# Performance work log

Hardware: AMD Instinct MI355X
Metric: run time of the kernel (lower is better)

The kernel has to match this reference:

```python
import jax, jax.numpy as jnp
import numpy as np

B, N, F_IN = 256, 256, 128
HID, DEPTH = 48, 4
D_OUT = 97                 # sum(latent_dim [32,32,32,1]) = GraphUNet out_channels
K_SORT = 30
C1, C2, KW2 = 16, 32, 5
POOL_LEN = (K_SORT - 2) // 2 + 1        # 15 after maxpool1d(2,2)
DENSE_DIM = (POOL_LEN - KW2 + 1) * C2   # 352
OUT_DIM = 32


def _gcn(x, A, W, b):
    # GCNConv(improved=True): A_hat = A + 2I; out = D^-1/2 A_hat D^-1/2 (x W) + b
    n = A.shape[-1]
    Ah = A + 2.0 * jnp.eye(n, dtype=A.dtype)
    dinv = jax.lax.rsqrt(jnp.sum(Ah, axis=-1))          # deg >= 2 always
    An = dinv[:, :, None] * Ah * dinv[:, None, :]
    return An @ (x @ W) + b


def _augment(A):
    # GraphUNet.augment_adj: add self loops, two-hop (A@A), remove self loops
    n = A.shape[-1]
    eye = jnp.eye(n, dtype=A.dtype)
    A1 = A + eye
    return (A1 @ A1) * (1.0 - eye)


def _topk_pool(x, A, p):
    # TopKPooling(ratio=0.5, nonlinearity=tanh): score = tanh(x.p/||p||)
    Bb, n, _ = x.shape
    score = jnp.tanh((x @ p) / jnp.sqrt(jnp.sum(p * p)))
    k = (n + 1) // 2
    vals, perm = jax.lax.top_k(score, k)                # [B,k]
    bidx = jnp.arange(Bb)[:, None]
    xp = x[bidx, perm] * vals[..., None]                # gate kept nodes by score
    Ap = A[bidx[..., None], perm[:, :, None], perm[:, None, :]]
    return xp, Ap, perm


def _forward(x, A, dW0, db0, dW, db, pool_p, uW, ub, uWl, ubl, c1W, c1b, c2W, c2b, oW, ob):
    act = jax.nn.relu
    # ---- GraphUNet down path ----
    h = act(_gcn(x, A, dW0, db0))
    xs, As, perms = [h], [A], []
    Acur = A
    for i in range(DEPTH):
        A2 = _augment(Acur)
        h, Acur, perm = _topk_pool(h, A2, pool_p[i])
        h = act(_gcn(h, Acur, dW[i], db[i]))
        if i < DEPTH - 1:
            xs.append(h)
            As.append(Acur)
        perms.append(perm)
    # ---- up path with sum skip connections ----
    for i in range(DEPTH):
        j = DEPTH - 1 - i
        res, Aj, perm = xs[j], As[j], perms[j]
        bidx = jnp.arange(res.shape[0])[:, None]
        up = jnp.zeros_like(res).at[bidx, perm].set(h)
        h = res + up
        if i < DEPTH - 1:
            h = act(_gcn(h, Aj, uW[i], ub[i]))
        else:
            h = _gcn(h, Aj, uWl, ubl)                   # [B,N,D_OUT], no act
    # ---- global_sort_pool: sort nodes by last channel desc, keep top K_SORT ----
    _, order = jax.lax.top_k(h[..., -1], K_SORT)
    sp = h[jnp.arange(B)[:, None], order]               # [B,K_SORT,D_OUT]
    # conv1d(1->C1, kernel=stride=D_OUT) on flattened [B,1,K*D] == per-node linear
    y = jax.nn.relu(jnp.einsum('bkd,cd->bck', sp, c1W) + c1b[None, :, None])  # [B,C1,K]
    y = y.reshape(B, C1, POOL_LEN, 2).max(-1)           # maxpool1d(2,2)
    y = jax.lax.conv_general_dilated(y, c2W, (1,), 'VALID',
                                     dimension_numbers=('NCH', 'OIH', 'NCH'))
    y = jax.nn.relu(y + c2b[None, :, None])             # [B,C2,POOL_LEN-KW2+1]
    return jax.nn.relu(y.reshape(B, -1) @ oW + ob)      # relu(relu(.)) == relu(.)


def setup_inputs():
    key = jax.random.key(0)
    ks = jax.random.split(key, 12)
    x = jax.random.normal(ks[0], (B, N, F_IN), dtype=jnp.float32)
    # symmetric binary adjacency, no self loops, avg degree ~15
    u = jax.random.uniform(ks[1], (B, N, N))
    A = (u < 0.03).astype(jnp.float32)
    A = jnp.maximum(A, A.transpose(0, 2, 1)) * (1.0 - jnp.eye(N, dtype=jnp.float32))
    s = lambda f: np.float32(1.0 / np.sqrt(f))
    return dict(
        x=x, A=A,
        dW0=jax.random.normal(ks[2], (F_IN, HID), dtype=jnp.float32) * s(F_IN),
        db0=jnp.zeros((HID,), jnp.float32),
        dW=jax.random.normal(ks[3], (DEPTH, HID, HID), dtype=jnp.float32) * s(HID),
        db=jnp.zeros((DEPTH, HID), jnp.float32),
        pool_p=jax.random.normal(ks[4], (DEPTH, HID), dtype=jnp.float32) * s(HID),
        uW=jax.random.normal(ks[5], (DEPTH - 1, HID, HID), dtype=jnp.float32) * s(HID),
        ub=jnp.zeros((DEPTH - 1, HID), jnp.float32),
        uWl=jax.random.normal(ks[6], (HID, D_OUT), dtype=jnp.float32) * s(HID),
        ubl=jnp.zeros((D_OUT,), jnp.float32),
        c1W=jax.random.normal(ks[7], (C1, D_OUT), dtype=jnp.float32) * s(D_OUT),
        c1b=jnp.zeros((C1,), jnp.float32),
        c2W=jax.random.normal(ks[8], (C2, C1, KW2), dtype=jnp.float32) * s(C1 * KW2),
        c2b=jnp.zeros((C2,), jnp.float32),
        oW=jax.random.normal(ks[9], (DENSE_DIM, OUT_DIM), dtype=jnp.float32) * s(DENSE_DIM),
        ob=jnp.zeros((OUT_DIM,), jnp.float32),
    )


def reference(x, A, dW0, db0, dW, db, pool_p, uW, ub, uWl, ubl, c1W, c1b, c2W, c2b, oW, ob):
    return _forward(x, A, dW0, db0, dW, db, pool_p, uW, ub, uWl, ubl, c1W, c1b, c2W, c2b, oW, ob)
```

## Files before the change

### kernel.cpp

```cpp
#include <hip/hip_runtime.h>
#include <math.h>

#define BATCH 256
#define NNODE 256
#define FIN   128
#define HID   48
#define DOUT  97

#define WOFF_DW0 0
#define WOFF_DW  6144
#define WOFF_UW  18432
#define WOFF_UWL 27648
#define WTOT     34816

typedef __attribute__((ext_vector_type(8))) short bf16x8_t;
typedef __attribute__((ext_vector_type(4))) float f32x4_t;

__device__ inline unsigned short f2bf(float x) {
  unsigned u = __float_as_uint(x);
  u += 0x7fff + ((u >> 16) & 1);
  return (unsigned short)(u >> 16);
}
__device__ inline float bf2f(unsigned short h) {
  return __uint_as_float(((unsigned)h) << 16);
}

template<int L> __device__ inline float grp_sum(float v) {
  #pragma unroll
  for (int o = L >> 1; o > 0; o >>= 1) v += __shfl_xor(v, o);
  return v;
}
template<int L> __device__ inline int grp_isum(int v) {
  #pragma unroll
  for (int o = L >> 1; o > 0; o >>= 1) v += __shfl_xor(v, o);
  return v;
}

__global__ __launch_bounds__(256) void k_prepA(const float* __restrict__ A,
                                               unsigned short* __restrict__ Abf,
                                               float* __restrict__ dinv, int rows) {
  int wid = (blockIdx.x * 256 + threadIdx.x) >> 6;
  int lane = threadIdx.x & 63;
  if (wid >= rows) return;
  const float4* rp = (const float4*)(A + (size_t)wid * 256);
  float4 v = rp[lane];
  unsigned long long pk = (unsigned long long)f2bf(v.x)
                        | ((unsigned long long)f2bf(v.y) << 16)
                        | ((unsigned long long)f2bf(v.z) << 32)
                        | ((unsigned long long)f2bf(v.w) << 48);
  *(unsigned long long*)(Abf + (size_t)wid * 256 + lane * 4) = pk;
  float s = v.x + v.y + v.z + v.w;
  #pragma unroll
  for (int o = 32; o > 0; o >>= 1) s += __shfl_down(s, o);
  if (lane == 0) dinv[wid] = 1.0f / sqrtf(s + 2.0f);
}

__global__ __launch_bounds__(256) void k_splitW3(const float* __restrict__ dW0,
                                                 const float* __restrict__ dW,
                                                 const float* __restrict__ uW,
                                                 const float* __restrict__ uWl,
                                                 unsigned short* __restrict__ Wp) {
  int idx = blockIdx.x * 256 + threadIdx.x;
  if (idx >= WTOT) return;
  float v;
  if (idx < WOFF_DW) {
    int f = idx / 128, kk = idx - f * 128;
    v = dW0[kk * HID + f];
  } else if (idx < WOFF_UW) {
    int r = idx - WOFF_DW;
    int i = r / 3072; r -= i * 3072;
    int f = r / 64, kk = r - f * 64;
    v = (kk < HID) ? dW[((size_t)i * HID + kk) * HID + f] : 0.f;
  } else if (idx < WOFF_UWL) {
    int r = idx - WOFF_UW;
    int i = r / 3072; r -= i * 3072;
    int f = r / 64, kk = r - f * 64;
    v = (kk < HID) ? uW[((size_t)i * HID + kk) * HID + f] : 0.f;
  } else {
    int r = idx - WOFF_UWL;
    int f = r / 64, kk = r - f * 64;
    v = (f < DOUT && kk < HID) ? uWl[(size_t)kk * DOUT + f] : 0.f;
  }
  unsigned short h = f2bf(v);
  float r1 = v - bf2f(h);
  unsigned short m = f2bf(r1);
  float r2 = r1 - bf2f(m);
  unsigned short l = f2bf(r2);
  Wp[idx] = h;
  Wp[idx + WTOT] = m;
  Wp[idx + 2 * WTOT] = l;
}

__global__ __launch_bounds__(1024) void k_big(const float* __restrict__ x,
                                              const unsigned short* __restrict__ Wp0,
                                              const unsigned short* __restrict__ Abf0,
                                              const float* __restrict__ D0,
                                              const float* __restrict__ db0,
                                              float* __restrict__ H0) {
  __shared__ __align__(16) char yt0[24576];
  __shared__ __align__(16) char yt1[24576];
  int b = blockIdx.x, t = threadIdx.x;
  int w = t >> 6, lane = t & 63;
  int r = lane & 15, q = lane >> 4;
  const float* Xb = x + (size_t)b * 256 * 128;
  const float* Db = D0 + (size_t)b * 256;
  {
    int m = w;
    const float* xr = Xb + (size_t)(m * 16 + r) * 128;
    bf16x8_t ah[4], am[4], al[4];
    #pragma unroll
    for (int ks = 0; ks < 4; ks++) {
      int col0 = ks * 32 + q * 8;
      float4 a4 = *(const float4*)(xr + col0);
      float4 b4 = *(const float4*)(xr + col0 + 4);
      float v[8] = {a4.x, a4.y, a4.z, a4.w, b4.x, b4.y, b4.z, b4.w};
      #pragma unroll
      for (int j = 0; j < 8; j++) {
        unsigned short h = f2bf(v[j]); float r1 = v[j] - bf2f(h);
        unsigned short mm = f2bf(r1);  float r2 = r1 - bf2f(mm);
        ah[ks][j] = (short)h; am[ks][j] = (short)mm; al[ks][j] = (short)f2bf(r2);
      }
    }
    int row0 = m * 16 + q * 4;
    float4 dv4 = *(const float4*)(Db + row0);
    float dvv[4] = {dv4.x, dv4.y, dv4.z, dv4.w};
    #pragma unroll
    for (int ft = 0; ft < 3; ft++) {
      int fl = ft * 16 + r;
      const unsigned short* wb = Wp0 + (size_t)fl * 128 + q * 8;
      f32x4_t acc = {0.f, 0.f, 0.f, 0.f};
      #pragma unroll
      for (int ks = 0; ks < 4; ks++) {
        bf16x8_t bh = *(const bf16x8_t*)(wb + ks * 32);
        bf16x8_t bm = *(const bf16x8_t*)(wb + WTOT + ks * 32);
        bf16x8_t bl = *(const bf16x8_t*)(wb + 2 * WTOT + ks * 32);
        acc = __builtin_amdgcn_mfma_f32_16x16x32_bf16(ah[ks], bh, acc, 0, 0, 0);
        acc = __builtin_amdgcn_mfma_f32_16x16x32_bf16(ah[ks], bm, acc, 0, 0, 0);
        acc = __builtin_amdgcn_mfma_f32_16x16x32_bf16(am[ks], bh, acc, 0, 0, 0);
        acc = __builtin_amdgcn_mfma_f32_16x16x32_bf16(am[ks], bm, acc, 0, 0, 0);
        acc = __builtin_amdgcn_mfma_f32_16x16x32_bf16(ah[ks], bl, acc, 0, 0, 0);
        acc = __builtin_amdgcn_mfma_f32_16x16x32_bf16(al[ks], bh, acc, 0, 0, 0);
      }
      #pragma unroll
      for (int reg = 0; reg < 4; reg++) {
        float vv = dvv[reg] * acc[reg];
        unsigned short hi = f2bf(vv);
        unsigned short lo = f2bf(vv - bf2f(hi));
        int byte = (fl * 512 + (row0 + reg) * 2) ^ ((fl & 7) << 4);
        *(unsigned short*)(yt0 + byte) = hi;
        *(unsigned short*)(yt1 + byte) = lo;
      }
    }
  }
  __syncthreads();
  {
    int it = w;
    const unsigned short* ap = Abf0 + ((size_t)b * 256 + it * 16 + r) * 256 + q * 8;
    bf16x8_t af[8];
    #pragma unroll
    for (int ks = 0; ks < 8; ks++) af[ks] = *(const bf16x8_t*)(ap + ks * 32);
    #pragma unroll
    for (int ft = 0; ft < 3; ft++) {
      int fl = ft * 16 + r;
      f32x4_t acc = {0.f, 0.f, 0.f, 0.f};
      #pragma unroll
      for (int ks = 0; ks < 8; ks++) {
        int byte = (fl * 512 + (ks * 32 + q * 8) * 2) ^ ((fl & 7) << 4);
        bf16x8_t bh = *(const bf16x8_t*)(yt0 + byte);
        bf16x8_t bl = *(const bf16x8_t*)(yt1 + byte);
        acc = __builtin_amdgcn_mfma_f32_16x16x32_bf16(af[ks], bh, acc, 0, 0, 0);
        acc = __builtin_amdgcn_mfma_f32_16x16x32_bf16(af[ks], bl, acc, 0, 0, 0);
      }
      float bfv = db0[fl];
      #pragma unroll
      for (int reg = 0; reg < 4; reg++) {
        int rr = it * 16 + q * 4 + reg;
        int sbyte = (fl * 512 + rr * 2) ^ ((fl & 7) << 4);
        float selfv = bf2f(*(const unsigned short*)(yt0 + sbyte))
                    + bf2f(*(const unsigned short*)(yt1 + sbyte));
        float d = Db[rr];
        float v = d * acc[reg] + 2.f * d * selfv + bfv;
        H0[((size_t)b * 256 + rr) * 48 + fl] = fmaxf(v, 0.f);
      }
    }
  }
}

template<int MODE>
__device__ inline void gcn128_phase(const float* __restrict__ Xg,
                                    const unsigned short* __restrict__ Wpl,
                                    const unsigned short* __restrict__ A1,
                                    const float* __restrict__ D1b,
                                    const float* __restrict__ bias,
                                    char* yt0, char* yt1,
                                    float* __restrict__ H1,
                                    float* __restrict__ H0b,
                                    const int* sPerm1, int t) {
  int w = t >> 6, lane = t & 63;
  int r = lane & 15, q = lane >> 4;
  for (int task = w; task < 24; task += 16) {
    int m = task / 3, ft = task - m * 3;
    const float* xr = Xg + (size_t)(m * 16 + r) * 48;
    bf16x8_t ah[2], am[2], al[2];
    #pragma unroll
    for (int ks = 0; ks < 2; ks++) {
      int col0 = ks * 32 + q * 8;
      float v[8];
      if (col0 + 8 <= 48) {
        float4 a4 = *(const float4*)(xr + col0);
        float4 b4 = *(const float4*)(xr + col0 + 4);
        v[0]=a4.x; v[1]=a4.y; v[2]=a4.z; v[3]=a4.w;
        v[4]=b4.x; v[5]=b4.y; v[6]=b4.z; v[7]=b4.w;
      } else {
        #pragma unroll
        for (int j = 0; j < 8; j++) v[j] = (col0 + j < 48) ? xr[col0 + j] : 0.f;
      }
      #pragma unroll
      for (int j = 0; j < 8; j++) {
        unsigned short h = f2bf(v[j]); float r1 = v[j] - bf2f(h);
        unsigned short mm = f2bf(r1);  float r2 = r1 - bf2f(mm);
        ah[ks][j] = (short)h; am[ks][j] = (short)mm; al[ks][j] = (short)f2bf(r2);
      }
    }
    int row0 = m * 16 + q * 4;
    float4 dv4 = *(const float4*)(D1b + row0);
    float dvv[4] = {dv4.x, dv4.y, dv4.z, dv4.w};
    int fl = ft * 16 + r;
    const unsigned short* wb = Wpl + (size_t)fl * 64 + q * 8;
    f32x4_t acc = {0.f, 0.f, 0.f, 0.f};
    #pragma unroll
    for (int ks = 0; ks < 2; ks++) {
      bf16x8_t bh = *(const bf16x8_t*)(wb + ks * 32);
      bf16x8_t bm = *(const bf16x8_t*)(wb + WTOT + ks * 32);
      bf16x8_t bl = *(const bf16x8_t*)(wb + 2 * WTOT + ks * 32);
      acc = __builtin_amdgcn_mfma_f32_16x16x32_bf16(ah[ks], bh, acc, 0, 0, 0);
      acc = __builtin_amdgcn_mfma_f32_16x16x32_bf16(ah[ks], bm, acc, 0, 0, 0);
      acc = __builtin_amdgcn_mfma_f32_16x16x32_bf16(am[ks], bh, acc, 0, 0, 0);
      acc = __builtin_amdgcn_mfma_f32_16x16x32_bf16(am[ks], bm, acc, 0, 0, 0);
      acc = __builtin_amdgcn_mfma_f32_16x16x32_bf16(ah[ks], bl, acc, 0, 0, 0);
      acc = __builtin_amdgcn_mfma_f32_16x16x32_bf16(al[ks], bh, acc, 0, 0, 0);
// ... 88 lines not shown
  for (int g = sub; g < 48; g += LPR) acc += hr[g] * p[g];
  acc = grp_sum<LPR>(acc);
  if (sub == 0) sS[row] = tanhf(acc / sqrtf(pn));
  __syncthreads();
  {
    float v = sS[row];
    int rk = 0;
    for (int j = sub; j < N; j += LPR) {
      float u = sS[j];
      rk += (u > v) || (u == v && j < row);
    }
    rk = grp_isum<LPR>(rk);
    if (sub == 0 && rk < K) perm[rk] = row;
  }
  __syncthreads();
  for (int idx = t; idx < K * 48; idx += 1024) {
    int r = idx / 48, g = idx - r * 48;
    int pi = perm[r];
    hin[idx] = h[pi * 48 + g] * sS[pi];
  }
  for (int idx = t; idx < K * K; idx += 1024) {
    int r = idx / K, c = idx - r * K;
    int pr = perm[r], pc = perm[c];
    const float* ra = A + pr * lda;
    const float* rc = A + pc * lda;
    float a2 = 0.f;
    #pragma unroll 4
    for (int j = 0; j < N; j++) a2 += ra[j] * rc[j];
    float v = a2 + 2.f * ra[pc];
    Ao[r * ldo + c] = (r == c) ? 0.f : v;
  }
  __syncthreads();
  {
    constexpr int LPR2 = 1024 / K;
    constexpr int LG = (LPR2 > 64 ? 64 : LPR2);
    int row2 = t / LPR2, sub2 = t % LPR2;
    float s = 0.f;
    for (int j = sub2; j < K; j += LPR2) s += Ao[row2 * ldo + j];
    s = grp_sum<LG>(s);
    if (sub2 == 0) dout[row2] = 1.0f / sqrtf(s + 2.0f);
  }
  __syncthreads();
}

__device__ inline void scat_phase(const int* perm, const float* src, float* dst,
                                  int k, int t) {
  for (int idx = t; idx < k * 48; idx += 1024) {
    int r = idx / 48, g = idx - r * 48;
    dst[perm[r] * 48 + g] += src[idx];
  }
  __syncthreads();
}

__global__ __launch_bounds__(1024) void k_mid(const unsigned short* __restrict__ Abf0,
                                              unsigned short* __restrict__ Abf1g,
                                              float* __restrict__ H0,
                                              float* __restrict__ H1g,
                                              float* __restrict__ D1g,
                                              const unsigned short* __restrict__ Wp,
                                              const float* __restrict__ dW,
                                              const float* __restrict__ dbv,
                                              const float* __restrict__ pp,
                                              const float* __restrict__ uW,
                                              const float* __restrict__ ub) {
  int b = blockIdx.x, t = threadIdx.x;
  __shared__ __align__(16) char arena[63488];
  __shared__ int sPerm1[128];
  float* H1 = H1g + (size_t)b * 128 * 48;
  float* H0b = H0 + (size_t)b * 256 * 48;
  unsigned short* A1 = Abf1g + (size_t)b * 128 * 128;
  float* D1b = D1g + (size_t)b * 128;

  {
    float* sc = (float*)arena;
    const float* p = pp;
    float pn = 0.f;
    #pragma unroll
    for (int g = 0; g < 48; g++) pn += p[g] * p[g];
    int row = t >> 2, sub = t & 3;
    const float* hr = H0b + (size_t)row * 48;
    float a = 0.f;
    for (int g = sub; g < 48; g += 4) a += hr[g] * p[g];
    a = grp_sum<4>(a);
    if (!sub) sc[row] = tanhf(a / sqrtf(pn));
    __syncthreads();
    float vv = sc[row];
    int rk = 0;
    for (int j = sub; j < 256; j += 4) {
      float u = sc[j];
      rk += (u > vv) || (u == vv && j < row);
    }
    rk = grp_isum<4>(rk);
    if (!sub && rk < 128) sPerm1[rk] = row;
  }
  __syncthreads();

  {
    float* sc = (float*)arena;
    for (int idx = t; idx < 128 * 48; idx += 1024) {
      int rr = idx / 48, g = idx - rr * 48;
      int pi = sPerm1[rr];
      H1[idx] = H0b[(size_t)pi * 48 + g] * sc[pi];
    }
    int w = t >> 6, lane = t & 63;
    int r = lane & 15, q = lane >> 4;
    int it = w >> 1, fh = w & 1;
    int rowA = sPerm1[it * 16 + r];
    const unsigned short* Ab = Abf0 + (size_t)b * 256 * 256;
    const unsigned short* pa = Ab + (size_t)rowA * 256 + q * 8;
    bf16x8_t af[8];
    #pragma unroll
    for (int ks = 0; ks < 8; ks++) {
      bf16x8_t a = *(const bf16x8_t*)(pa + ks * 32);
      int da = rowA - ks * 32 - q * 8;
      #pragma unroll
      for (int e = 0; e < 8; e++) if (da == e) a[e] = (short)0x3F80;
      af[ks] = a;
    }
    for (int ft = fh * 4; ft < fh * 4 + 4; ft++) {
      int rowB = sPerm1[ft * 16 + r];
      const unsigned short* pb = Ab + (size_t)rowB * 256 + q * 8;
      f32x4_t acc = {0.f, 0.f, 0.f, 0.f};
      #pragma unroll
      for (int ks = 0; ks < 8; ks++) {
        bf16x8_t bv = *(const bf16x8_t*)(pb + ks * 32);
        int db_ = rowB - ks * 32 - q * 8;
        #pragma unroll
        for (int e = 0; e < 8; e++) if (db_ == e) bv[e] = (short)0x3F80;
        acc = __builtin_amdgcn_mfma_f32_16x16x32_bf16(af[ks], bv, acc, 0, 0, 0);
      }
      int c = ft * 16 + r;
      #pragma unroll
      for (int reg = 0; reg < 4; reg++) {
        int rr = it * 16 + q * 4 + reg;
        float v = (rr == c) ? 0.f : acc[reg];
        A1[(size_t)rr * 128 + c] = f2bf(v);
      }
    }
  }
  __syncthreads();
  {
    int row = t >> 3, sub = t & 7;
    const unsigned* ar = (const unsigned*)(A1 + (size_t)row * 128);
    float s = 0.f;
    for (int jj = sub; jj < 64; jj += 8) {
      unsigned u = ar[jj];
      s += bf2f((unsigned short)(u & 0xffffu)) + bf2f((unsigned short)(u >> 16));
    }
    s = grp_sum<8>(s);
    if (sub == 0) D1b[row] = 1.0f / sqrtf(s + 2.0f);
  }
  __syncthreads();

  gcn128_phase<0>(H1, Wp + WOFF_DW, A1, D1b, dbv,
                  (char*)arena, (char*)arena + 12288, H1, nullptr, sPerm1, t);

  {
    float* sS  = (float*)(arena);
    int*   sP2 = (int*)(arena + 512);
    int*   sP3 = (int*)(arena + 768);
    int*   sP4 = (int*)(arena + 896);
    float* sD2 = (float*)(arena + 960);
    float* sD3 = (float*)(arena + 1216);
    float* sD4 = (float*)(arena + 1344);
    float* sA2 = (float*)(arena + 1536);
    float* sA3 = (float*)(arena + 18176);
    float* sH2 = (float*)(arena + 22400);
    float* sH3 = (float*)(arena + 34688);
    float* sXW = (float*)(arena + 40832);
    float* hin = (float*)(arena + 53120);
    float* sH4 = (float*)(arena + 59264);
    float* sA4 = (float*)(arena + 62336);

    {
      const float* p = pp + 48;
      float pn = 0.f;
      #pragma unroll
      for (int g = 0; g < 48; g++) pn += p[g] * p[g];
      int row = t >> 3, sub = t & 7;
      const float* hr = H1 + (size_t)row * 48;
      float acc = 0.f;
      for (int g = sub; g < 48; g += 8) acc += hr[g] * p[g];
      acc = grp_sum<8>(acc);
      if (sub == 0) sS[row] = tanhf(acc / sqrtf(pn));
      __syncthreads();
      float v = sS[row];
      int rk = 0;
      for (int j = sub; j < 128; j += 8) {
        float u = sS[j];
        rk += (u > v) || (u == v && j < row);
      }
      rk = grp_isum<8>(rk);
      if (sub == 0 && rk < 64) sP2[rk] = row;
      __syncthreads();
    }
    {
      int w = t >> 6, lane = t & 63;
      int r = lane & 15, q = lane >> 4;
      int it = w >> 2, ft = w & 3;
      int rowA = sP2[it * 16 + r];
      int rowB = sP2[ft * 16 + r];
      const unsigned short* pa = A1 + (size_t)rowA * 128 + q * 8;
      const unsigned short* pb = A1 + (size_t)rowB * 128 + q * 8;
      f32x4_t acc = {0.f, 0.f, 0.f, 0.f};
      #pragma unroll
      for (int k0 = 0; k0 < 128; k0 += 32) {
        bf16x8_t a  = *(const bf16x8_t*)(pa + k0);
        bf16x8_t bv = *(const bf16x8_t*)(pb + k0);
        int daA = rowA - k0 - q * 8;
        int daB = rowB - k0 - q * 8;
        #pragma unroll
        for (int e = 0; e < 8; e++) {
          if (daA == e) a[e] = (short)0x3F80;
          if (daB == e) bv[e] = (short)0x3F80;
        }
        acc = __builtin_amdgcn_mfma_f32_16x16x32_bf16(a, bv, acc, 0, 0, 0);
      }
      int c = ft * 16 + r;
      #pragma unroll
      for (int reg = 0; reg < 4; reg++) {
        int rr = it * 16 + q * 4 + reg;
        sA2[rr * 65 + c] = (rr == c) ? 0.f : acc[reg];
      }
    }
    __syncthreads();
    {
      int row = t >> 4, sub = t & 15;
      float s = 0.f;
      for (int j = sub; j < 64; j += 16) s += sA2[row * 65 + j];
      s = grp_sum<16>(s);
      if (sub == 0) sD2[row] = 1.0f / sqrtf(s + 2.0f);
    }
    __syncthreads();
    for (int idx = t; idx < 64 * 48; idx += 1024) {
      int j = idx / 48, f = idx - j * 48;
      int pi = sP2[j];
      const float* hr = H1 + (size_t)pi * 48;
      const float* W = dW + 2304;
      float a = 0.f;
      #pragma unroll
      for (int g = 0; g < 48; g++) a += hr[g] * W[g * 48 + f];
      sXW[idx] = sD2[j] * sS[pi] * a;
    }
    __syncthreads();
    anxw_phase(sA2, 65, sXW, sD2, dbv + 48, sH2, 64, t);
    __syncthreads();

    pool_aug_phaseT<64, 32>(sH2, pp + 96, sA2, 65, sA3, 33, sS, sP3, hin, sD3, t);
    xw_dphase(hin, dW + 2 * 2304, sD3, sXW, 32, t);
    __syncthreads();
    anxw_phase(sA3, 33, sXW, sD3, dbv + 96, sH3, 32, t);
    __syncthreads();

    pool_aug_phaseT<32, 16>(sH3, pp + 144, sA3, 33, sA4, 17, sS, sP4, hin, sD4, t);
    xw_dphase(hin, dW + 3 * 2304, sD4, sXW, 16, t);
    __syncthreads();
    anxw_phase(sA4, 17, sXW, sD4, dbv + 144, sH4, 16, t);
    __syncthreads();

    scat_phase(sP4, sH4, sH3, 16, t);
    xw_dphase(sH3, uW, sD3, sXW, 32, t);
    __syncthreads();
    anxw_phase(sA3, 33, sXW, sD3, ub, sH3, 32, t);
    __syncthreads();

    scat_phase(sP3, sH3, sH2, 32, t);
    xw_dphase(sH2, uW + 2304, sD2, sXW, 64, t);
    __syncthreads();
    anxw_phase(sA2, 65, sXW, sD2, ub + 48, sH2, 64, t);
    __syncthreads();

    for (int idx = t; idx < 64 * 48; idx += 1024) {
      int r2 = idx / 48, g = idx - r2 * 48;
      H1[(size_t)sP2[r2] * 48 + g] += sH2[idx];
    }
  }
  __syncthreads();

  gcn128_phase<1>(H1, Wp + WOFF_UW + 2 * 3072, A1, D1b, ub + 96,
                  (char*)arena, (char*)arena + 12288, nullptr, H0b, sPerm1, t);
}

__global__ __launch_bounds__(1024) void k_tail(const float* __restrict__ H0,
                                               const unsigned short* __restrict__ Wpl,
                                               const unsigned short* __restrict__ Abf,
                                               const float* __restrict__ dinv,
                                               const float* __restrict__ ubl,
                                               float* __restrict__ sp) {
  int b = blockIdx.x, t = threadIdx.x;
  __shared__ float ydt[16][257];
  __shared__ float sc[256];
  __shared__ int sord[32];
  int w = t >> 6, lane = t & 63;
  int r = lane & 15, q = lane >> 4;
  const float* H0b = H0 + (size_t)b * 256 * 48;
  const float* Db = dinv + (size_t)b * 256;

  bf16x8_t ah[2], am[2], al[2];
  {
    const float* xr = H0b + (size_t)(w * 16 + r) * 48;
    #pragma unroll
    for (int ks = 0; ks < 2; ks++) {
      int col0 = ks * 32 + q * 8;
      float v[8];
      if (col0 + 8 <= 48) {
        float4 a4 = *(const float4*)(xr + col0);
        float4 b4 = *(const float4*)(xr + col0 + 4);
        v[0]=a4.x; v[1]=a4.y; v[2]=a4.z; v[3]=a4.w;
        v[4]=b4.x; v[5]=b4.y; v[6]=b4.z; v[7]=b4.w;
      } else {
        #pragma unroll
        for (int j = 0; j < 8; j++) v[j] = (col0 + j < 48) ? xr[col0 + j] : 0.f;
      }
      #pragma unroll
      for (int j = 0; j < 8; j++) {
        unsigned short h = f2bf(v[j]); float r1 = v[j] - bf2f(h);
        unsigned short mm = f2bf(r1);  float r2 = r1 - bf2f(mm);
        ah[ks][j] = (short)h; am[ks][j] = (short)mm; al[ks][j] = (short)f2bf(r2);
      }
    }
  }
  int row0 = w * 16 + q * 4;
  float4 dv4 = *(const float4*)(Db + row0);
  float dvv[4] = {dv4.x, dv4.y, dv4.z, dv4.w};

  auto stepA = [&](int ft) {
    int fl = ft * 16 + r;
    const unsigned short* wb = Wpl + (size_t)fl * 64 + q * 8;
    f32x4_t acc = {0.f, 0.f, 0.f, 0.f};
    #pragma unroll
    for (int ks = 0; ks < 2; ks++) {
      bf16x8_t bh = *(const bf16x8_t*)(wb + ks * 32);
      bf16x8_t bm = *(const bf16x8_t*)(wb + WTOT + ks * 32);
      bf16x8_t bl = *(const bf16x8_t*)(wb + 2 * WTOT + ks * 32);
      acc = __builtin_amdgcn_mfma_f32_16x16x32_bf16(ah[ks], bh, acc, 0, 0, 0);
      acc = __builtin_amdgcn_mfma_f32_16x16x32_bf16(ah[ks], bm, acc, 0, 0, 0);
      acc = __builtin_amdgcn_mfma_f32_16x16x32_bf16(am[ks], bh, acc, 0, 0, 0);
      acc = __builtin_amdgcn_mfma_f32_16x16x32_bf16(am[ks], bm, acc, 0, 0, 0);
      acc = __builtin_amdgcn_mfma_f32_16x16x32_bf16(ah[ks], bl, acc, 0, 0, 0);
      acc = __builtin_amdgcn_mfma_f32_16x16x32_bf16(al[ks], bh, acc, 0, 0, 0);
    }
    #pragma unroll
    for (int reg = 0; reg < 4; reg++)
      ydt[r][row0 + reg] = dvv[reg] * acc[reg];
  };

  auto stepB = [&](int ft, int nf) {
    int o = t >> 1, sub = t & 1;
    if (o < 30 * nf) {
      int rr = o / nf, f = o - rr * nf;
      int fl = ft * 16 + f;
      int node = sord[rr];
      const unsigned short* ar = Abf + ((size_t)b * 256 + node) * 256 + sub * 128;
      const float* yp = &ydt[f][sub * 128];
      float s = 0.f;
      for (int j = 0; j < 128; j += 2) {
        unsigned u = *(const unsigned*)(ar + j);
        s += bf2f((unsigned short)(u & 0xffffu)) * yp[j]
           + bf2f((unsigned short)(u >> 16)) * yp[j + 1];
      }
      s += __shfl_xor(s, 1);
      if (!sub) {
        float d = Db[node];
        sp[((size_t)b * 30 + rr) * DOUT + fl] = d * s + 2.f * d * ydt[f][node] + ubl[fl];
      }
    }
  };

  stepA(6);
  __syncthreads();
  {
    int i = t >> 2, sub = t & 3;
    const unsigned short* ar = Abf + ((size_t)b * 256 + i) * 256 + sub * 64;
    const float* yp = &ydt[0][sub * 64];
    float s = 0.f;
    for (int j = 0; j < 64; j += 2) {
      unsigned u = *(const unsigned*)(ar + j);
      s += bf2f((unsigned short)(u & 0xffffu)) * yp[j]
         + bf2f((unsigned short)(u >> 16)) * yp[j + 1];
    }
    s = grp_sum<4>(s);
    if (!sub) {
      float d = Db[i];
      sc[i] = d * s + 2.f * d * ydt[0][i];
    }
  }
  __syncthreads();
  {
    int i = t >> 2, sub = t & 3;
    float v = sc[i];
    int rk = 0;
    int j0 = sub * 64;
    for (int j = j0; j < j0 + 64; j++) {
      float u = sc[j];
      rk += (u > v) || (u == v && j < i);
    }
    rk = grp_isum<4>(rk);
    if (!sub && rk < 30) sord[rk] = i;
  }
  __syncthreads();
  stepB(6, 1);
  __syncthreads();
  for (int ft = 0; ft < 6; ft++) {
    stepA(ft);
    __syncthreads();
    stepB(ft, 16);
    __syncthreads();
  }
}

__global__ __launch_bounds__(256) void k_head2(const float* __restrict__ spg,
                                               const float* __restrict__ c1W,
                                               const float* __restrict__ c1b,
                                               const float* __restrict__ c2W,
                                               const float* __restrict__ c2b,
                                               const float* __restrict__ oW,
                                               const float* __restrict__ ob,
                                               float* __restrict__ out) {
  int b = blockIdx.x, t = threadIdx.x;
  __shared__ float sp[30 * 97];
  __shared__ float y1[16 * 30];
  __shared__ float yp[16 * 15];
  __shared__ float yc[32 * 11];
  __shared__ float red[256];
  const float* spb = spg + (size_t)b * 30 * 97;
  for (int idx = t; idx < 30 * 97; idx += 256) sp[idx] = spb[idx];
  __syncthreads();
  for (int idx = t; idx < 16 * 30; idx += 256) {
    int c = idx / 30, kk = idx - c * 30;
    float a = c1b[c];
    for (int d = 0; d < 97; d++) a += sp[kk * 97 + d] * c1W[c * 97 + d];
    y1[c * 30 + kk] = fmaxf(a, 0.f);
  }
  __syncthreads();
  for (int idx = t; idx < 16 * 15; idx += 256) {
    int c = idx / 15, t2 = idx - c * 15;
    yp[idx] = fmaxf(y1[c * 30 + 2 * t2], y1[c * 30 + 2 * t2 + 1]);
  }
  __syncthreads();
  for (int idx = t; idx < 32 * 11; idx += 256) {
    int o = idx / 11, t3 = idx - o * 11;
    float a = c2b[o];
    for (int i2 = 0; i2 < 16; i2++)
      for (int w = 0; w < 5; w++)
        a += yp[i2 * 15 + t3 + w] * c2W[(o * 16 + i2) * 5 + w];
    yc[o * 11 + t3] = fmaxf(a, 0.f);
  }
  __syncthreads();
  {
    int o = t & 31, g = t >> 5;
    float a = 0.f;
    for (int qq = g * 44; qq < g * 44 + 44; qq++) a += yc[qq] * oW[qq * 32 + o];
    red[t] = a;
  }
  __syncthreads();
  if (t < 32) {
    float a = ob[t];
    #pragma unroll
    for (int g = 0; g < 8; g++) a += red[t + 32 * g];
    out[(size_t)b * 32 + t] = fmaxf(a, 0.f);
  }
}

extern "C" void kernel_launch(void* const* d_in, const int* in_sizes, int n_in,
                              void* d_out, int out_size, void* d_ws, size_t ws_size,
                              hipStream_t stream) {
  const float* x   = (const float*)d_in[0];
  const float* A0  = (const float*)d_in[1];
  const float* dW0 = (const float*)d_in[2];
  const float* db0 = (const float*)d_in[3];
  const float* dW  = (const float*)d_in[4];
  const float* dbv = (const float*)d_in[5];
  const float* pp  = (const float*)d_in[6];
  const float* uW  = (const float*)d_in[7];
  const float* ub  = (const float*)d_in[8];
  const float* uWl = (const float*)d_in[9];
  const float* ubl = (const float*)d_in[10];
  const float* c1W = (const float*)d_in[11];
  const float* c1b = (const float*)d_in[12];
  const float* c2W = (const float*)d_in[13];
  const float* c2b = (const float*)d_in[14];
  const float* oW  = (const float*)d_in[15];
  const float* ob  = (const float*)d_in[16];
  float* out = (float*)d_out;

  float* base = (float*)d_ws;
  size_t off = 0;
  auto alloc = [&](size_t nel) { nel = (nel + 3) & ~(size_t)3; float* p = base + off; off += nel; return p; };
  float* H0 = alloc((size_t)BATCH * 256 * HID);
  float* H1 = alloc((size_t)BATCH * 128 * HID);
  float* D0 = alloc((size_t)BATCH * 256);
  float* D1 = alloc((size_t)BATCH * 128);
  float* SP = alloc((size_t)BATCH * 30 * 97);
  unsigned short* Abf0 = (unsigned short*)alloc((size_t)BATCH * 256 * 256 / 2);
  unsigned short* Abf1 = (unsigned short*)alloc((size_t)BATCH * 128 * 128 / 2);
  unsigned short* Wp   = (unsigned short*)alloc((size_t)3 * WTOT / 2 + 4);

  k_prepA<<<BATCH * 256 / 4, 256, 0, stream>>>(A0, Abf0, D0, BATCH * 256);
  k_splitW3<<<(WTOT + 255) / 256, 256, 0, stream>>>(dW0, dW, uW, uWl, Wp);

  k_big<<<BATCH, 1024, 0, stream>>>(x, Wp + WOFF_DW0, Abf0, D0, db0, H0);

  k_mid<<<BATCH, 1024, 0, stream>>>(Abf0, Abf1, H0, H1, D1, Wp, dW, dbv, pp, uW, ub);

  k_tail<<<BATCH, 1024, 0, stream>>>(H0, Wp + WOFF_UWL, Abf0, D0, ubl, SP);

  k_head2<<<BATCH, 256, 0, stream>>>(SP, c1W, c1b, c2W, c2b, oW, ob, out);
}
```

Baseline: 360.5 us.

## Fuse A-prep, first GCN, mid, tail and head kernels into one per-graph kernel

```diff
diff --git a/kernel.cpp b/kernel.cpp
--- a/kernel.cpp
+++ b/kernel.cpp
@@ -34,25 +34,6 @@
   #pragma unroll
   for (int o = L >> 1; o > 0; o >>= 1) v += __shfl_xor(v, o);
   return v;
-}
-
-__global__ __launch_bounds__(256) void k_prepA(const float* __restrict__ A,
-                                               unsigned short* __restrict__ Abf,
-                                               float* __restrict__ dinv, int rows) {
-  int wid = (blockIdx.x * 256 + threadIdx.x) >> 6;
-  int lane = threadIdx.x & 63;
-  if (wid >= rows) return;
-  const float4* rp = (const float4*)(A + (size_t)wid * 256);
-  float4 v = rp[lane];
-  unsigned long long pk = (unsigned long long)f2bf(v.x)
-                        | ((unsigned long long)f2bf(v.y) << 16)
-                        | ((unsigned long long)f2bf(v.z) << 32)
-                        | ((unsigned long long)f2bf(v.w) << 48);
-  *(unsigned long long*)(Abf + (size_t)wid * 256 + lane * 4) = pk;
-  float s = v.x + v.y + v.z + v.w;
-  #pragma unroll
-  for (int o = 32; o > 0; o >>= 1) s += __shfl_down(s, o);
-  if (lane == 0) dinv[wid] = 1.0f / sqrtf(s + 2.0f);
 }
 
 __global__ __launch_bounds__(256) void k_splitW3(const float* __restrict__ dW0,
@@ -91,101 +72,6 @@
   Wp[idx + 2 * WTOT] = l;
 }
 
-__global__ __launch_bounds__(1024) void k_big(const float* __restrict__ x,
-                                              const unsigned short* __restrict__ Wp0,
-                                              const unsigned short* __restrict__ Abf0,
-                                              const float* __restrict__ D0,
-                                              const float* __restrict__ db0,
-                                              float* __restrict__ H0) {
-  __shared__ __align__(16) char yt0[24576];
-  __shared__ __align__(16) char yt1[24576];
-  int b = blockIdx.x, t = threadIdx.x;
-  int w = t >> 6, lane = t & 63;
-  int r = lane & 15, q = lane >> 4;
-  const float* Xb = x + (size_t)b * 256 * 128;
-  const float* Db = D0 + (size_t)b * 256;
-  {
-    int m = w;
-    const float* xr = Xb + (size_t)(m * 16 + r) * 128;
-    bf16x8_t ah[4], am[4], al[4];
-    #pragma unroll
-    for (int ks = 0; ks < 4; ks++) {
-      int col0 = ks * 32 + q * 8;
-      float4 a4 = *(const float4*)(xr + col0);
-      float4 b4 = *(const float4*)(xr + col0 + 4);
-      float v[8] = {a4.x, a4.y, a4.z, a4.w, b4.x, b4.y, b4.z, b4.w};
-      #pragma unroll
-      for (int j = 0; j < 8; j++) {
-        unsigned short h = f2bf(v[j]); float r1 = v[j] - bf2f(h);
-        unsigned short mm = f2bf(r1);  float r2 = r1 - bf2f(mm);
-        ah[ks][j] = (short)h; am[ks][j] = (short)mm; al[ks][j] = (short)f2bf(r2);
-      }
-    }
-    int row0 = m * 16 + q * 4;
-    float4 dv4 = *(const float4*)(Db + row0);
-    float dvv[4] = {dv4.x, dv4.y, dv4.z, dv4.w};
-    #pragma unroll
-    for (int ft = 0; ft < 3; ft++) {
-      int fl = ft * 16 + r;
-      const unsigned short* wb = Wp0 + (size_t)fl * 128 + q * 8;
-      f32x4_t acc = {0.f, 0.f, 0.f, 0.f};
-      #pragma unroll
-      for (int ks = 0; ks < 4; ks++) {
-        bf16x8_t bh = *(const bf16x8_t*)(wb + ks * 32);
-        bf16x8_t bm = *(const bf16x8_t*)(wb + WTOT + ks * 32);
-        bf16x8_t bl = *(const bf16x8_t*)(wb + 2 * WTOT + ks * 32);
-        acc = __builtin_amdgcn_mfma_f32_16x16x32_bf16(ah[ks], bh, acc, 0, 0, 0);
-        acc = __builtin_amdgcn_mfma_f32_16x16x32_bf16(ah[ks], bm, acc, 0, 0, 0);
-        acc = __builtin_amdgcn_mfma_f32_16x16x32_bf16(am[ks], bh, acc, 0, 0, 0);
-        acc = __builtin_amdgcn_mfma_f32_16x16x32_bf16(am[ks], bm, acc, 0, 0, 0);
-        acc = __builtin_amdgcn_mfma_f32_16x16x32_bf16(ah[ks], bl, acc, 0, 0, 0);
-        acc = __builtin_amdgcn_mfma_f32_16x16x32_bf16(al[ks], bh, acc, 0, 0, 0);
-      }
-      #pragma unroll
-      for (int reg = 0; reg < 4; reg++) {
-        float vv = dvv[reg] * acc[reg];
-        unsigned short hi = f2bf(vv);
-        unsigned short lo = f2bf(vv - bf2f(hi));
-        int byte = (fl * 512 + (row0 + reg) * 2) ^ ((fl & 7) << 4);
-        *(unsigned short*)(yt0 + byte) = hi;
-        *(unsigned short*)(yt1 + byte) = lo;
-      }
-    }
-  }
-  __syncthreads();
-  {
-    int it = w;
-    const unsigned short* ap = Abf0 + ((size_t)b * 256 + it * 16 + r) * 256 + q * 8;
-    bf16x8_t af[8];
-    #pragma unroll
-    for (int ks = 0; ks < 8; ks++) af[ks] = *(const bf16x8_t*)(ap + ks * 32);
-    #pragma unroll
-    for (int ft = 0; ft < 3; ft++) {
-      int fl = ft * 16 + r;
-      f32x4_t acc = {0.f, 0.f, 0.f, 0.f};
-      #pragma unroll
-      for (int ks = 0; ks < 8; ks++) {
-        int byte = (fl * 512 + (ks * 32 + q * 8) * 2) ^ ((fl & 7) << 4);
-        bf16x8_t bh = *(const bf16x8_t*)(yt0 + byte);
-        bf16x8_t bl = *(const bf16x8_t*)(yt1 + byte);
-        acc = __builtin_amdgcn_mfma_f32_16x16x32_bf16(af[ks], bh, acc, 0, 0, 0);
-        acc = __builtin_amdgcn_mfma_f32_16x16x32_bf16(af[ks], bl, acc, 0, 0, 0);
-      }
-      float bfv = db0[fl];
-      #pragma unroll
-      for (int reg = 0; reg < 4; reg++) {
-        int rr = it * 16 + q * 4 + reg;
-        int sbyte = (fl * 512 + rr * 2) ^ ((fl & 7) << 4);
-        float selfv = bf2f(*(const unsigned short*)(yt0 + sbyte))
-                    + bf2f(*(const unsigned short*)(yt1 + sbyte));
-        float d = Db[rr];
-        float v = d * acc[reg] + 2.f * d * selfv + bfv;
-        H0[((size_t)b * 256 + rr) * 48 + fl] = fmaxf(v, 0.f);
-      }
-    }
-  }
-}
-
 template<int MODE>
 __device__ inline void gcn128_phase(const float* __restrict__ Xg,
                                     const unsigned short* __restrict__ Wpl,
@@ -380,24 +266,134 @@
   __syncthreads();
 }
 
-__global__ __launch_bounds__(1024) void k_mid(const unsigned short* __restrict__ Abf0,
-                                              unsigned short* __restrict__ Abf1g,
-                                              float* __restrict__ H0,
-                                              float* __restrict__ H1g,
-                                              float* __restrict__ D1g,
-                                              const unsigned short* __restrict__ Wp,
-                                              const float* __restrict__ dW,
-                                              const float* __restrict__ dbv,
-                                              const float* __restrict__ pp,
-                                              const float* __restrict__ uW,
-                                              const float* __restrict__ ub) {
+__global__ __launch_bounds__(1024) void k_gunet(
+    const float* __restrict__ x, const float* __restrict__ A0,
+    const unsigned short* __restrict__ Wp,
+    const float* __restrict__ db0, const float* __restrict__ dW,
+    const float* __restrict__ dbv, const float* __restrict__ pp,
+    const float* __restrict__ uW, const float* __restrict__ ub,
+    const float* __restrict__ ubl,
+    const float* __restrict__ c1W, const float* __restrict__ c1b,
+    const float* __restrict__ c2W, const float* __restrict__ c2b,
+    const float* __restrict__ oW, const float* __restrict__ ob,
+    unsigned short* __restrict__ Abf0g, unsigned short* __restrict__ Abf1g,
+    float* __restrict__ H0g, float* __restrict__ H1g, float* __restrict__ D1g,
+    float* __restrict__ out) {
   int b = blockIdx.x, t = threadIdx.x;
   __shared__ __align__(16) char arena[63488];
   __shared__ int sPerm1[128];
+  __shared__ __align__(16) float sD0[256];
+
+  const float* A0b = A0 + (size_t)b * 65536;
+  unsigned short* Ab = Abf0g + (size_t)b * 65536;
+  float* H0b = H0g + (size_t)b * 256 * 48;
   float* H1 = H1g + (size_t)b * 128 * 48;
-  float* H0b = H0 + (size_t)b * 256 * 48;
   unsigned short* A1 = Abf1g + (size_t)b * 128 * 128;
   float* D1b = D1g + (size_t)b * 128;
+  int w = t >> 6, lane = t & 63;
+  int r = lane & 15, q = lane >> 4;
+
+  for (int row = w; row < 256; row += 16) {
+    const float4* rp = (const float4*)(A0b + (size_t)row * 256);
+    float4 v = rp[lane];
+    unsigned long long pk = (unsigned long long)f2bf(v.x)
+                          | ((unsigned long long)f2bf(v.y) << 16)
+                          | ((unsigned long long)f2bf(v.z) << 32)
+                          | ((unsigned long long)f2bf(v.w) << 48);
+    *(unsigned long long*)(Ab + (size_t)row * 256 + lane * 4) = pk;
+    float s = v.x + v.y + v.z + v.w;
+    #pragma unroll
+    for (int o = 32; o > 0; o >>= 1) s += __shfl_down(s, o);
+    if (lane == 0) sD0[row] = 1.0f / sqrtf(s + 2.0f);
+  }
+  __syncthreads();
+
+  {
+    char* yt0 = arena;
+    char* yt1 = arena + 24576;
+    const float* Xb = x + (size_t)b * 256 * 128;
+    {
+      int m = w;
+      const float* xr = Xb + (size_t)(m * 16 + r) * 128;
+      bf16x8_t ah[4], am[4], al[4];
+      #pragma unroll
+      for (int ks = 0; ks < 4; ks++) {
+        int col0 = ks * 32 + q * 8;
+        float4 a4 = *(const float4*)(xr + col0);
+        float4 b4 = *(const float4*)(xr + col0 + 4);
+        float v[8] = {a4.x, a4.y, a4.z, a4.w, b4.x, b4.y, b4.z, b4.w};
+        #pragma unroll
+        for (int j = 0; j < 8; j++) {
+          unsigned short h = f2bf(v[j]); float r1 = v[j] - bf2f(h);
+          unsigned short mm = f2bf(r1);  float r2 = r1 - bf2f(mm);
+          ah[ks][j] = (short)h; am[ks][j] = (short)mm; al[ks][j] = (short)f2bf(r2);
+        }
+      }
+      int row0 = m * 16 + q * 4;
+      float4 dv4 = *(const float4*)(sD0 + row0);
+      float dvv[4] = {dv4.x, dv4.y, dv4.z, dv4.w};
+      #pragma unroll
+      for (int ft = 0; ft < 3; ft++) {
+        int fl = ft * 16 + r;
+        const unsigned short* wb = Wp + WOFF_DW0 + (size_t)fl * 128 + q * 8;
+        f32x4_t acc = {0.f, 0.f, 0.f, 0.f};
+        #pragma unroll
+        for (int ks = 0; ks < 4; ks++) {
+          bf16x8_t bh = *(const bf16x8_t*)(wb + ks * 32);
+          bf16x8_t bm = *(const bf16x8_t*)(wb + WTOT + ks * 32);
+          bf16x8_t bl = *(const bf16x8_t*)(wb + 2 * WTOT + ks * 32);
+          acc = __builtin_amdgcn_mfma_f32_16x16x32_bf16(ah[ks], bh, acc, 0, 0, 0);
+          acc = __builtin_amdgcn_mfma_f32_16x16x32_bf16(ah[ks], bm, acc, 0, 0, 0);
+          acc = __builtin_amdgcn_mfma_f32_16x16x32_bf16(am[ks], bh, acc, 0, 0, 0);
+          acc = __builtin_amdgcn_mfma_f32_16x16x32_bf16(am[ks], bm, acc, 0, 0, 0);
+          acc = __builtin_amdgcn_mfma_f32_16x16x32_bf16(ah[ks], bl, acc, 0, 0, 0);
+          acc = __builtin_amdgcn_mfma_f32_16x16x32_bf16(al[ks], bh, acc, 0, 0, 0);
+        }
+        #pragma unroll
+        for (int reg = 0; reg < 4; reg++) {
+          float vv = dvv[reg] * acc[reg];
+          unsigned short hi = f2bf(vv);
+          unsigned short lo = f2bf(vv - bf2f(hi));
+          int byte = (fl * 512 + (row0 + reg) * 2) ^ ((fl & 7) << 4);
+          *(unsigned short*)(yt0 + byte) = hi;
+          *(unsigned short*)(yt1 + byte) = lo;
+        }
+      }
+    }
+    __syncthreads();
+    {
+      int it = w;
+      const unsigned short* ap = Ab + (size_t)(it * 16 + r) * 256 + q * 8;
+      bf16x8_t af[8];
+      #pragma unroll
+      for (int ks = 0; ks < 8; ks++) af[ks] = *(const bf16x8_t*)(ap + ks * 32);
+      #pragma unroll
+      for (int ft = 0; ft < 3; ft++) {
+        int fl = ft * 16 + r;
+        f32x4_t acc = {0.f, 0.f, 0.f, 0.f};
+        #pragma unroll
+        for (int ks = 0; ks < 8; ks++) {
+          int byte = (fl * 512 + (ks * 32 + q * 8) * 2) ^ ((fl & 7) << 4);
+          bf16x8_t bh = *(const bf16x8_t*)(yt0 + byte);
+          bf16x8_t bl = *(const bf16x8_t*)(yt1 + byte);
+          acc = __builtin_amdgcn_mfma_f32_16x16x32_bf16(af[ks], bh, acc, 0, 0, 0);
+          acc = __builtin_amdgcn_mfma_f32_16x16x32_bf16(af[ks], bl, acc, 0, 0, 0);
+        }
+        float bfv = db0[fl];
+        #pragma unroll
+        for (int reg = 0; reg < 4; reg++) {
+          int rr = it * 16 + q * 4 + reg;
+          int sbyte = (fl * 512 + rr * 2) ^ ((fl & 7) << 4);
+          float selfv = bf2f(*(const unsigned short*)(yt0 + sbyte))
+                      + bf2f(*(const unsigned short*)(yt1 + sbyte));
+          float d = sD0[rr];
+          float v = d * acc[reg] + 2.f * d * selfv + bfv;
+          H0b[(size_t)rr * 48 + fl] = fmaxf(v, 0.f);
+        }
+      }
+    }
+  }
+  __syncthreads();
 
   {
     float* sc = (float*)arena;
@@ -430,11 +426,8 @@
       int pi = sPerm1[rr];
       H1[idx] = H0b[(size_t)pi * 48 + g] * sc[pi];
     }
-    int w = t >> 6, lane = t & 63;
-    int r = lane & 15, q = lane >> 4;
     int it = w >> 1, fh = w & 1;
     int rowA = sPerm1[it * 16 + r];
-    const unsigned short* Ab = Abf0 + (size_t)b * 256 * 256;
     const unsigned short* pa = Ab + (size_t)rowA * 256 + q * 8;
     bf16x8_t af[8];
     #pragma unroll
@@ -481,7 +474,7 @@
   __syncthreads();
 
   gcn128_phase<0>(H1, Wp + WOFF_DW, A1, D1b, dbv,
-                  (char*)arena, (char*)arena + 12288, H1, nullptr, sPerm1, t);
+                  arena, arena + 12288, H1, nullptr, sPerm1, t);
 
   {
     float* sS  = (float*)(arena);
@@ -523,8 +516,6 @@
       __syncthreads();
     }
     {
-      int w = t >> 6, lane = t & 63;
-      int r = lane & 15, q = lane >> 4;
       int it = w >> 2, ft = w & 3;
       int rowA = sP2[it * 16 + r];
       int rowB = sP2[ft * 16 + r];
@@ -606,187 +597,166 @@
   __syncthreads();
 
   gcn128_phase<1>(H1, Wp + WOFF_UW + 2 * 3072, A1, D1b, ub + 96,
-                  (char*)arena, (char*)arena + 12288, nullptr, H0b, sPerm1, t);
-}
-
-__global__ __launch_bounds__(1024) void k_tail(const float* __restrict__ H0,
-                                               const unsigned short* __restrict__ Wpl,
-                                               const unsigned short* __restrict__ Abf,
-                                               const float* __restrict__ dinv,
-                                               const float* __restrict__ ubl,
-                                               float* __restrict__ sp) {
-  int b = blockIdx.x, t = threadIdx.x;
-  __shared__ float ydt[16][257];
-  __shared__ float sc[256];
-  __shared__ int sord[32];
-  int w = t >> 6, lane = t & 63;
-  int r = lane & 15, q = lane >> 4;
-  const float* H0b = H0 + (size_t)b * 256 * 48;
-  const float* Db = dinv + (size_t)b * 256;
-
-  bf16x8_t ah[2], am[2], al[2];
+                  arena, arena + 12288, nullptr, H0b, sPerm1, t);
+
+  float* spl = (float*)(arena + 16448);
   {
-    const float* xr = H0b + (size_t)(w * 16 + r) * 48;
-    #pragma unroll
-    for (int ks = 0; ks < 2; ks++) {
-      int col0 = ks * 32 + q * 8;
-      float v[8];
-      if (col0 + 8 <= 48) {
-        float4 a4 = *(const float4*)(xr + col0);
-        float4 b4 = *(const float4*)(xr + col0 + 4);
-        v[0]=a4.x; v[1]=a4.y; v[2]=a4.z; v[3]=a4.w;
-        v[4]=b4.x; v[5]=b4.y; v[6]=b4.z; v[7]=b4.w;
-      } else {
+    float* ydt = (float*)arena;
+    float* scp = (float*)(arena + 28096);
+    int* sord  = (int*)(arena + 29120);
+
+    bf16x8_t ah[2], am[2], al[2];
+    {
+      const float* xr = H0b + (size_t)(w * 16 + r) * 48;
+      #pragma unroll
+      for (int ks = 0; ks < 2; ks++) {
+        int col0 = ks * 32 + q * 8;
+        float v[8];
+        if (col0 + 8 <= 48) {
+          float4 a4 = *(const float4*)(xr + col0);
+          float4 b4 = *(const float4*)(xr + col0 + 4);
+          v[0]=a4.x; v[1]=a4.y; v[2]=a4.z; v[3]=a4.w;
+          v[4]=b4.x; v[5]=b4.y; v[6]=b4.z; v[7]=b4.w;
+        } else {
+          #pragma unroll
+          for (int j = 0; j < 8; j++) v[j] = (col0 + j < 48) ? xr[col0 + j] : 0.f;
+        }
         #pragma unroll
-        for (int j = 0; j < 8; j++) v[j] = (col0 + j < 48) ? xr[col0 + j] : 0.f;
-      }
-      #pragma unroll
-      for (int j = 0; j < 8; j++) {
-        unsigned short h = f2bf(v[j]); float r1 = v[j] - bf2f(h);
-        unsigned short mm = f2bf(r1);  float r2 = r1 - bf2f(mm);
-        ah[ks][j] = (short)h; am[ks][j] = (short)mm; al[ks][j] = (short)f2bf(r2);
-      }
-    }
-  }
-  int row0 = w * 16 + q * 4;
-  float4 dv4 = *(const float4*)(Db + row0);
-  float dvv[4] = {dv4.x, dv4.y, dv4.z, dv4.w};
-
-  auto stepA = [&](int ft) {
-    int fl = ft * 16 + r;
-    const unsigned short* wb = Wpl + (size_t)fl * 64 + q * 8;
-    f32x4_t acc = {0.f, 0.f, 0.f, 0.f};
-    #pragma unroll
-    for (int ks = 0; ks < 2; ks++) {
-      bf16x8_t bh = *(const bf16x8_t*)(wb + ks * 32);
-      bf16x8_t bm = *(const bf16x8_t*)(wb + WTOT + ks * 32);
-      bf16x8_t bl = *(const bf16x8_t*)(wb + 2 * WTOT + ks * 32);
-      acc = __builtin_amdgcn_mfma_f32_16x16x32_bf16(ah[ks], bh, acc, 0, 0, 0);
-      acc = __builtin_amdgcn_mfma_f32_16x16x32_bf16(ah[ks], bm, acc, 0, 0, 0);
-      acc = __builtin_amdgcn_mfma_f32_16x16x32_bf16(am[ks], bh, acc, 0, 0, 0);
-      acc = __builtin_amdgcn_mfma_f32_16x16x32_bf16(am[ks], bm, acc, 0, 0, 0);
-      acc = __builtin_amdgcn_mfma_f32_16x16x32_bf16(ah[ks], bl, acc, 0, 0, 0);
-      acc = __builtin_amdgcn_mfma_f32_16x16x32_bf16(al[ks], bh, acc, 0, 0, 0);
-    }
-    #pragma unroll
-    for (int reg = 0; reg < 4; reg++)
-      ydt[r][row0 + reg] = dvv[reg] * acc[reg];
-  };
-
-  auto stepB = [&](int ft, int nf) {
-    int o = t >> 1, sub = t & 1;
-    if (o < 30 * nf) {
-      int rr = o / nf, f = o - rr * nf;
-      int fl = ft * 16 + f;
-      int node = sord[rr];
-      const unsigned short* ar = Abf + ((size_t)b * 256 + node) * 256 + sub * 128;
-      const float* yp = &ydt[f][sub * 128];
+        for (int j = 0; j < 8; j++) {
+          unsigned short h = f2bf(v[j]); float r1 = v[j] - bf2f(h);
+          unsigned short mm = f2bf(r1);  float r2 = r1 - bf2f(mm);
+          ah[ks][j] = (short)h; am[ks][j] = (short)mm; al[ks][j] = (short)f2bf(r2);
+        }
+      }
+    }
+    int row0 = w * 16 + q * 4;
+    float4 dv4 = *(const float4*)(sD0 + row0);
+    float dvv[4] = {dv4.x, dv4.y, dv4.z, dv4.w};
+
+    auto stepA = [&](int ft) {
+      int fl = ft * 16 + r;
+      const unsigned short* wb = Wp + WOFF_UWL + (size_t)fl * 64 + q * 8;
+      f32x4_t acc = {0.f, 0.f, 0.f, 0.f};
+      #pragma unroll
+      for (int ks = 0; ks < 2; ks++) {
+        bf16x8_t bh = *(const bf16x8_t*)(wb + ks * 32);
+        bf16x8_t bm = *(const bf16x8_t*)(wb + WTOT + ks * 32);
+        bf16x8_t bl = *(const bf16x8_t*)(wb + 2 * WTOT + ks * 32);
+        acc = __builtin_amdgcn_mfma_f32_16x16x32_bf16(ah[ks], bh, acc, 0, 0, 0);
+        acc = __builtin_amdgcn_mfma_f32_16x16x32_bf16(ah[ks], bm, acc, 0, 0, 0);
+        acc = __builtin_amdgcn_mfma_f32_16x16x32_bf16(am[ks], bh, acc, 0, 0, 0);
+        acc = __builtin_amdgcn_mfma_f32_16x16x32_bf16(am[ks], bm, acc, 0, 0, 0);
+        acc = __builtin_amdgcn_mfma_f32_16x16x32_bf16(ah[ks], bl, acc, 0, 0, 0);
+        acc = __builtin_amdgcn_mfma_f32_16x16x32_bf16(al[ks], bh, acc, 0, 0, 0);
+      }
+      #pragma unroll
+      for (int reg = 0; reg < 4; reg++)
+        ydt[r * 257 + row0 + reg] = dvv[reg] * acc[reg];
+    };
+
+    auto stepB = [&](int ft, int nf) {
+      int o = t >> 1, sub = t & 1;
+      if (o < 30 * nf) {
+        int rr = o / nf, f = o - rr * nf;
+        int fl = ft * 16 + f;
+        int node = sord[rr];
+        const unsigned short* ar = Ab + (size_t)node * 256 + sub * 128;
+        const float* yp = &ydt[f * 257 + sub * 128];
+        float s = 0.f;
+        for (int j = 0; j < 128; j += 2) {
+          unsigned u = *(const unsigned*)(ar + j);
+          s += bf2f((unsigned short)(u & 0xffffu)) * yp[j]
+             + bf2f((unsigned short)(u >> 16)) * yp[j + 1];
+        }
+        s += __shfl_xor(s, 1);
+        if (!sub) {
+          float d = sD0[node];
+          spl[rr * DOUT + fl] = d * s + 2.f * d * ydt[f * 257 + node] + ubl[fl];
+        }
+      }
+    };
+
+    stepA(6);
+    __syncthreads();
+    {
+      int i = t >> 2, sub = t & 3;
+      const unsigned short* ar = Ab + (size_t)i * 256 + sub * 64;
+      const float* yp = &ydt[0 * 257 + sub * 64];
       float s = 0.f;
-      for (int j = 0; j < 128; j += 2) {
+      for (int j = 0; j < 64; j += 2) {
         unsigned u = *(const unsigned*)(ar + j);
         s += bf2f((unsigned short)(u & 0xffffu)) * yp[j]
            + bf2f((unsigned short)(u >> 16)) * yp[j + 1];
       }
-      s += __shfl_xor(s, 1);
+      s = grp_sum<4>(s);
       if (!sub) {
-        float d = Db[node];
-        sp[((size_t)b * 30 + rr) * DOUT + fl] = d * s + 2.f * d * ydt[f][node] + ubl[fl];
-      }
-    }
-  };
-
-  stepA(6);
-  __syncthreads();
+        float d = sD0[i];
+        scp[i] = d * s + 2.f * d * ydt[0 * 257 + i];
+      }
+    }
+    __syncthreads();
+    {
+      int i = t >> 2, sub = t & 3;
+      float v = scp[i];
+      int rk = 0;
+      int j0 = sub * 64;
+      for (int j = j0; j < j0 + 64; j++) {
+        float u = scp[j];
+        rk += (u > v) || (u == v && j < i);
+      }
+      rk = grp_isum<4>(rk);
+      if (!sub && rk < 30) sord[rk] = i;
+    }
+    __syncthreads();
+    stepB(6, 1);
+    __syncthreads();
+    for (int ft = 0; ft < 6; ft++) {
+      stepA(ft);
+      __syncthreads();
+      stepB(ft, 16);
+      __syncthreads();
+    }
+  }
+
   {
-    int i = t >> 2, sub = t & 3;
-    const unsigned short* ar = Abf + ((size_t)b * 256 + i) * 256 + sub * 64;
-    const float* yp = &ydt[0][sub * 64];
-    float s = 0.f;
-    for (int j = 0; j < 64; j += 2) {
-      unsigned u = *(const unsigned*)(ar + j);
-      s += bf2f((unsigned short)(u & 0xffffu)) * yp[j]
-         + bf2f((unsigned short)(u >> 16)) * yp[j + 1];
-    }
-    s = grp_sum<4>(s);
-    if (!sub) {
-      float d = Db[i];
-      sc[i] = d * s + 2.f * d * ydt[0][i];
-    }
-  }
-  __syncthreads();
-  {
-    int i = t >> 2, sub = t & 3;
-    float v = sc[i];
-    int rk = 0;
-    int j0 = sub * 64;
-    for (int j = j0; j < j0 + 64; j++) {
-      float u = sc[j];
-      rk += (u > v) || (u == v && j < i);
-    }
-    rk = grp_isum<4>(rk);
-    if (!sub && rk < 30) sord[rk] = i;
-  }
-  __syncthreads();
-  stepB(6, 1);
-  __syncthreads();
-  for (int ft = 0; ft < 6; ft++) {
-    stepA(ft);
-    __syncthreads();
-    stepB(ft, 16);
-    __syncthreads();
-  }
-}
-
-__global__ __launch_bounds__(256) void k_head2(const float* __restrict__ spg,
-                                               const float* __restrict__ c1W,
-                                               const float* __restrict__ c1b,
-                                               const float* __restrict__ c2W,
-                                               const float* __restrict__ c2b,
-                                               const float* __restrict__ oW,
-                                               const float* __restrict__ ob,
-                                               float* __restrict__ out) {
-  int b = blockIdx.x, t = threadIdx.x;
-  __shared__ float sp[30 * 97];
-  __shared__ float y1[16 * 30];
-  __shared__ float yp[16 * 15];
-  __shared__ float yc[32 * 11];
-  __shared__ float red[256];
-  const float* spb = spg + (size_t)b * 30 * 97;
-  for (int idx = t; idx < 30 * 97; idx += 256) sp[idx] = spb[idx];
-  __syncthreads();
-  for (int idx = t; idx < 16 * 30; idx += 256) {
-    int c = idx / 30, kk = idx - c * 30;
-    float a = c1b[c];
-    for (int d = 0; d < 97; d++) a += sp[kk * 97 + d] * c1W[c * 97 + d];
-    y1[c * 30 + kk] = fmaxf(a, 0.f);
-  }
-  __syncthreads();
-  for (int idx = t; idx < 16 * 15; idx += 256) {
-    int c = idx / 15, t2 = idx - c * 15;
-    yp[idx] = fmaxf(y1[c * 30 + 2 * t2], y1[c * 30 + 2 * t2 + 1]);
-  }
-  __syncthreads();
-  for (int idx = t; idx < 32 * 11; idx += 256) {
-    int o = idx / 11, t3 = idx - o * 11;
-    float a = c2b[o];
-    for (int i2 = 0; i2 < 16; i2++)
-      for (int w = 0; w < 5; w++)
-        a += yp[i2 * 15 + t3 + w] * c2W[(o * 16 + i2) * 5 + w];
-    yc[o * 11 + t3] = fmaxf(a, 0.f);
-  }
-  __syncthreads();
-  {
-    int o = t & 31, g = t >> 5;
-    float a = 0.f;
-    for (int qq = g * 44; qq < g * 44 + 44; qq++) a += yc[qq] * oW[qq * 32 + o];
-    red[t] = a;
-  }
-  __syncthreads();
-  if (t < 32) {
-    float a = ob[t];
-    #pragma unroll
-    for (int g = 0; g < 8; g++) a += red[t + 32 * g];
-    out[(size_t)b * 32 + t] = fmaxf(a, 0.f);
+    float* y1  = (float*)(arena + 32768);
+    float* yp  = (float*)(arena + 34688);
+    float* yc  = (float*)(arena + 35648);
+    float* red = (float*)(arena + 37056);
+    for (int idx = t; idx < 16 * 30; idx += 1024) {
+      int c = idx / 30, kk = idx - c * 30;
+      float a = c1b[c];
+      for (int d = 0; d < 97; d++) a += spl[kk * 97 + d] * c1W[c * 97 + d];
+      y1[c * 30 + kk] = fmaxf(a, 0.f);
+    }
+    __syncthreads();
+    for (int idx = t; idx < 16 * 15; idx += 1024) {
+      int c = idx / 15, t2 = idx - c * 15;
+      yp[idx] = fmaxf(y1[c * 30 + 2 * t2], y1[c * 30 + 2 * t2 + 1]);
+    }
+    __syncthreads();
+    for (int idx = t; idx < 32 * 11; idx += 1024) {
+      int o = idx / 11, t3 = idx - o * 11;
+      float a = c2b[o];
+      for (int i2 = 0; i2 < 16; i2++)
+        for (int ww = 0; ww < 5; ww++)
+          a += yp[i2 * 15 + t3 + ww] * c2W[(o * 16 + i2) * 5 + ww];
+      yc[o * 11 + t3] = fmaxf(a, 0.f);
+    }
+    __syncthreads();
+    {
+      int o = t & 31, g = t >> 5;
+      float a = 0.f;
+      for (int qq = g * 11; qq < g * 11 + 11; qq++) a += yc[qq] * oW[qq * 32 + o];
+      red[t] = a;
+    }
+    __syncthreads();
+    if (t < 32) {
+      float a = ob[t];
+      #pragma unroll
+      for (int g = 0; g < 32; g++) a += red[t + 32 * g];
+      out[(size_t)b * 32 + t] = fmaxf(a, 0.f);
+    }
   }
 }
 
@@ -817,21 +787,14 @@
   auto alloc = [&](size_t nel) { nel = (nel + 3) & ~(size_t)3; float* p = base + off; off += nel; return p; };
   float* H0 = alloc((size_t)BATCH * 256 * HID);
   float* H1 = alloc((size_t)BATCH * 128 * HID);
-  float* D0 = alloc((size_t)BATCH * 256);
   float* D1 = alloc((size_t)BATCH * 128);
-  float* SP = alloc((size_t)BATCH * 30 * 97);
   unsigned short* Abf0 = (unsigned short*)alloc((size_t)BATCH * 256 * 256 / 2);
   unsigned short* Abf1 = (unsigned short*)alloc((size_t)BATCH * 128 * 128 / 2);
   unsigned short* Wp   = (unsigned short*)alloc((size_t)3 * WTOT / 2 + 4);
 
-  k_prepA<<<BATCH * 256 / 4, 256, 0, stream>>>(A0, Abf0, D0, BATCH * 256);
   k_splitW3<<<(WTOT + 255) / 256, 256, 0, stream>>>(dW0, dW, uW, uWl, Wp);
 
-  k_big<<<BATCH, 1024, 0, stream>>>(x, Wp + WOFF_DW0, Abf0, D0, db0, H0);
-
-  k_mid<<<BATCH, 1024, 0, stream>>>(Abf0, Abf1, H0, H1, D1, Wp, dW, dbv, pp, uW, ub);
-
-  k_tail<<<BATCH, 1024, 0, stream>>>(H0, Wp + WOFF_UWL, Abf0, D0, ubl, SP);
-
-  k_head2<<<BATCH, 256, 0, stream>>>(SP, c1W, c1b, c2W, c2b, oW, ob, out);
-}
+  k_gunet<<<BATCH, 1024, 0, stream>>>(x, A0, Wp, db0, dW, dbv, pp, uW, ub, ubl,
+                                      c1W, c1b, c2W, c2b, oW, ob,
+                                      Abf0, Abf1, H0, H1, D1, out);
+}
```

Result: slower. 377.8 us (+4.8%).
